# Optimization experiments

Measured on AMD Instinct MI355X. Metric: run time of the kernel, lower is better.

The kernel has to match this reference:

```python
import jax, jax.numpy as jnp
import numpy as np

N = 50000
E = 800000
D = 128          # in_dim = hid_dim = out_dim
R = 8            # num_rels
B = 8            # num_bases
N_LAYERS = 2


def _rgcn_conv(x, basis, comp, root, bias, src, dst, etype):
    """One PyG-style RGCNConv with basis decomposition, mean aggregation per
    relation, root (self-loop) weight and bias.
    x: [N, Din]; basis: [B, Din, Dout]; comp: [R, B]; root: [Din, Dout]; bias: [Dout].
    """
    n = x.shape[0]
    # Relation weights from basis decomposition: W[r] = sum_b comp[r,b] * basis[b]
    W = jnp.einsum('rb,bio->rio', comp, basis)           # [R, Din, Dout]
    # Transform every node under every relation, then gather per-edge message.
    H = jnp.einsum('ni,rio->nro', x, W)                  # [N, R, Dout]
    msg = H[src, etype]                                  # [E, Dout]
    # Per-(dst, relation) in-degree for mean aggregation (PyG aggr='mean').
    deg = jnp.zeros((n, R), x.dtype).at[dst, etype].add(1.0)
    inv = 1.0 / jnp.maximum(deg[dst, etype], 1.0)        # [E]
    agg = jnp.zeros((n, W.shape[2]), x.dtype).at[dst].add(msg * inv[:, None])
    return agg + x @ root + bias


def setup_inputs() -> dict:
    key = jax.random.key(0)
    ks = jax.random.split(key, 3 + 4 * N_LAYERS)
    x = jax.random.normal(ks[0], (N, D), dtype=jnp.float32)
    edge_index = jax.random.randint(ks[1], (2, E), 0, N, dtype=jnp.int64)
    edge_type = jax.random.randint(ks[2], (E,), 0, R, dtype=jnp.int64)
    inp = {'x': x, 'edge_index': edge_index, 'edge_type': edge_type}
    scale = 1.0 / np.sqrt(D)
    for l in range(N_LAYERS):
        k0, k1, k2 = ks[3 + 4 * l], ks[4 + 4 * l], ks[5 + 4 * l]
        inp[f'basis{l}'] = jax.random.normal(k0, (B, D, D), dtype=jnp.float32) * scale
        inp[f'comp{l}'] = jax.random.normal(k1, (R, B), dtype=jnp.float32) * (1.0 / np.sqrt(B))
        inp[f'root{l}'] = jax.random.normal(k2, (D, D), dtype=jnp.float32) * scale
        inp[f'bias{l}'] = jnp.zeros((D,), dtype=jnp.float32)
    return inp


def reference(x, edge_index, edge_type,
              basis0, comp0, root0, bias0,
              basis1, comp1, root1, bias1):
    src, dst = edge_index[0], edge_index[1]
    etype = edge_type
    h = _rgcn_conv(x, basis0, comp0, root0, bias0, src, dst, etype)
    h = jax.nn.relu(h)                 # activation between layers (dropout=0.0)
    h = _rgcn_conv(h, basis1, comp1, root1, bias1, src, dst, etype)
    return h
```

## Files before the change

### kernel.cpp

```cpp
#include <hip/hip_runtime.h>

#define NN 50000
#define EE 800000
#define DD 128
#define RR 8
#define KSTACK 1152
#define NR2 (NN * RR)
#define RPB 16
#define ROWB 2304
#define DUMPB 36864u
#define DUMP16 2304

typedef __attribute__((ext_vector_type(8))) short bf16x8;
typedef __attribute__((ext_vector_type(4))) float f32x4;

__device__ inline float bf2f(ushort u) {
    union { uint i; float f; } v; v.i = ((uint)u) << 16; return v.f;
}
__device__ inline ushort f2bf(float f) {
    uint b = __float_as_uint(f);
    uint r = (b + 0x7fffu + ((b >> 16) & 1u)) >> 16;
    return (ushort)r;
}

__global__ void __launch_bounds__(256) k_build_w3(
        const float* __restrict__ b0, const float* __restrict__ c0,
        const float* __restrict__ r0, const float* __restrict__ b1,
        const float* __restrict__ c1, const float* __restrict__ r1,
        ushort* __restrict__ w0, ushort* __restrict__ w1) {
    __shared__ float tile[32][132];
    const float* basis = blockIdx.y ? b1 : b0;
    const float* comp  = blockIdx.y ? c1 : c0;
    const float* root  = blockIdx.y ? r1 : r0;
    ushort* wT         = blockIdx.y ? w1 : w0;
    int tid = threadIdx.x;
    int k0 = blockIdx.x * 32;
    #pragma unroll
    for (int it = 0; it < 16; ++it) {
        int idx = it * 256 + tid;
        int kk = idx >> 7, o = idx & 127;
        int k = k0 + kk;
        float val;
        if (k < RR * DD) {
            int r = k >> 7, i = k & 127;
            float s = 0.f;
            #pragma unroll
            for (int b = 0; b < 8; ++b) s += comp[r * 8 + b] * basis[(b * 128 + i) * 128 + o];
            val = s;
        } else {
            val = root[(k - RR * DD) * 128 + o];
        }
        tile[kk][o] = val;
    }
    __syncthreads();
    int o = tid >> 1, half = tid & 1;
    ushort* wp = wT + (size_t)o * KSTACK + k0 + half * 16;
    #pragma unroll
    for (int j = 0; j < 8; ++j) {
        float lo = tile[half * 16 + 2 * j][o];
        float hi = tile[half * 16 + 2 * j + 1][o];
        uint pk;
        asm("v_cvt_pk_bf16_f32 %0, %1, %2" : "=v"(pk) : "v"(lo), "v"(hi));
        *(uint*)(wp + 2 * j) = pk;
    }
}

__global__ void k_cvt_bf16(const float* __restrict__ x, ushort* __restrict__ xb, int n4) {
    int i = blockIdx.x * 256 + threadIdx.x;
    if (i < n4) {
        float4 v = ((const float4*)x)[i];
        uint2 p;
        p.x = (uint)f2bf(v.x) | ((uint)f2bf(v.y) << 16);
        p.y = (uint)f2bf(v.z) | ((uint)f2bf(v.w) << 16);
        ((uint2*)xb)[i] = p;
    }
}

__global__ void k_hist(const int* __restrict__ ei, const int* __restrict__ et,
                       int* __restrict__ deg_dr) {
    int e = blockIdx.x * 256 + threadIdx.x;
    if (e < EE) atomicAdd(&deg_dr[ei[EE + e] * RR + et[e]], 1);
}

__device__ inline int rowdeg(const int* __restrict__ deg_dr, int n) {
    int4 a = ((const int4*)deg_dr)[2 * n];
    int4 b = ((const int4*)deg_dr)[2 * n + 1];
    return a.x + a.y + a.z + a.w + b.x + b.y + b.z + b.w;
}

__global__ void k_scan1(const int* __restrict__ deg_dr, int* __restrict__ bsum, int n) {
    __shared__ int s[256];
    int t = threadIdx.x;
    int i = blockIdx.x * 256 + t;
    s[t] = (i < n) ? rowdeg(deg_dr, i) : 0;
    __syncthreads();
    for (int o = 128; o > 0; o >>= 1) {
        if (t < o) s[t] += s[t + o];
        __syncthreads();
    }
    if (t == 0) bsum[blockIdx.x] = s[0];
}

__global__ void k_scan2(int* __restrict__ bsum, int nb) {
    __shared__ int s[256];
    int t = threadIdx.x;
    int v = (t < nb) ? bsum[t] : 0;
    s[t] = v;
    __syncthreads();
    for (int o = 1; o < 256; o <<= 1) {
        int u = (t >= o) ? s[t - o] : 0;
        __syncthreads();
        s[t] += u;
        __syncthreads();
    }
    if (t < nb) bsum[t] = s[t] - v;
}

__global__ void k_scan3(const int* __restrict__ deg_dr, const int* __restrict__ boff,
                        int* __restrict__ ptr, int n) {
    __shared__ int s[256];
    int t = threadIdx.x;
    int i = blockIdx.x * 256 + t;
    int v = (i < n) ? rowdeg(deg_dr, i) : 0;
    s[t] = v;
    __syncthreads();
    for (int o = 1; o < 256; o <<= 1) {
        int u = (t >= o) ? s[t - o] : 0;
        __syncthreads();
        s[t] += u;
        __syncthreads();
    }
    if (i < n) ptr[i + 1] = boff[blockIdx.x] + s[t];
    if (i == 0) ptr[0] = 0;
}

__global__ void k_scatter(const int* __restrict__ ei, const int* __restrict__ et,
                          const int* __restrict__ row_ptr, const int* __restrict__ deg_dr,
                          int* __restrict__ cursor, int2* __restrict__ ekw) {
    int e = blockIdx.x * 256 + threadIdx.x;
    if (e < EE) {
        int s = ei[e], d = ei[EE + e], t = et[e];
        int4 a = ((const int4*)deg_dr)[2 * d];
        int4 b = ((const int4*)deg_dr)[2 * d + 1];
        int pre = 0;
        pre += (t > 0) ? a.x : 0; pre += (t > 1) ? a.y : 0;
        pre += (t > 2) ? a.z : 0; pre += (t > 3) ? a.w : 0;
        pre += (t > 4) ? b.x : 0; pre += (t > 5) ? b.y : 0;
        pre += (t > 6) ? b.z : 0;
        int deg = (t == 0) ? a.x : (t == 1) ? a.y : (t == 2) ? a.z : (t == 3) ? a.w
                : (t == 4) ? b.x : (t == 5) ? b.y : (t == 6) ? b.z : b.w;
        int p = row_ptr[d] + pre + atomicAdd(&cursor[d * RR + t], 1);
        int lrow = d & (RPB - 1);
        int base16 = lrow * (ROWB >> 4) + t * 16;
        int2 pk;
        pk.x = (base16 << 19) | ((lrow & 7) << 16) | s;
        pk.y = __float_as_int(1.f / (float)deg);
        ekw[p] = pk;
    }
}

__global__ void __launch_bounds__(512, 4) k_fused8(
        const ushort* __restrict__ in, const int* __restrict__ rp,
        const int2* __restrict__ ekw, const ushort* __restrict__ BT,
        const float* __restrict__ bias, ushort* __restrict__ hout,
        float* __restrict__ fout) {
    __shared__ uint4 at4[(RPB * ROWB + 256) / 16];
    char* atb = (char*)at4;
    int tid = threadIdx.x, wid = tid >> 6, lane = tid & 63;
    int blockrow = blockIdx.x * RPB;
    uint lane4 = (uint)lane << 2;

    {
        uint4 z = {0u, 0u, 0u, 0u};
        for (int i = tid; i < (RPB * ROWB + 256) / 16; i += 512) at4[i] = z;
    }
    __syncthreads();

    const ushort* inl = in + (lane << 1);

    #pragma unroll
    for (int rr = 0; rr < 2; ++rr) {
        int lr = (wid << 1) + rr;
        int n = blockrow + lr;
        uint su = *(const uint*)(inl + (size_t)n * DD);
        uint off = (uint)(lr * ROWB + 2048) + (lane4 ^ ((uint)(lr & 7) << 4));
        *(uint*)(atb + off) = su;
    }

    int n0 = blockrow + (wid << 1);
    int p    = __builtin_amdgcn_readfirstlane(rp[n0]);
    int pend = __builtin_amdgcn_readfirstlane(rp[n0 + 2]);
    int nb = pend - p;

    const int U = 8;
    int2 kA[U], kB[U];
    uint gA[U], gB[U];
    float a0 = 0.f, a1 = 0.f;
    uint prev = 0xFFFFFFFFu;

    auto loadc = [&](int2* kb, uint* gb, int base) {
        #pragma unroll
        for (int j = 0; j < U; ++j) {
            int pe = base + j;
            bool dummy = pe >= pend;
            pe = dummy ? (pend - 1) : pe;
            int2 e = ekw[pe];
            if (dummy) { e.x = (int)((uint)DUMP16 << 19); e.y = 0; }
            kb[j] = e;
        }
        #pragma unroll
        for (int j = 0; j < U; ++j)
            gb[j] = *(const uint*)(inl + ((size_t)(kb[j].x & 0xFFFF)) * DD);
    };
    auto proc = [&](int2* kb, uint* gb) {
        #pragma unroll
        for (int j = 0; j < U; ++j) {
            uint ex = (uint)kb[j].x;
            float w = __int_as_float(kb[j].y);
            uint off = ((ex >> 19) << 4) + (lane4 ^ ((ex >> 12) & 0x70u));
            bool same = (off == prev);
            a0 = same ? a0 : 0.f;
            a1 = same ? a1 : 0.f;
            uint g = gb[j];
            a0 += w * bf2f((ushort)(g & 0xFFFFu));
            a1 += w * bf2f((ushort)(g >> 16));
            uint pk;
            asm("v_cvt_pk_bf16_f32 %0, %1, %2" : "=v"(pk) : "v"(a0), "v"(a1));
            *(uint*)(atb + off) = pk;
            prev = off;
        }
    };

    if (nb > 0) {
        int nch = (nb + U - 1) / U;
        loadc(kA, gA, p);
        int i = 1;
        for (; i + 1 < nch; i += 2) {
            loadc(kB, gB, p + i * U);
            proc(kA, gA);
            loadc(kA, gA, p + (i + 1) * U);
            proc(kB, gB);
        }
        if (i < nch) {
            loadc(kB, gB, p + i * U);
            proc(kA, gA);
            proc(kB, gB);
        } else {
            proc(kA, gA);
        }
    }
    __syncthreads();

    int rlo = lane & 15, q = lane >> 4;
    int colbase = wid << 4;
    uint x7 = (uint)(rlo & 7) << 4;
    const char* arow = atb + rlo * ROWB;
    const ushort* bp = BT + (size_t)(colbase + rlo) * KSTACK + (q << 3);
    f32x4 c0 = {0.f, 0.f, 0.f, 0.f};
    #pragma unroll 4
    for (int kk = 0; kk < KSTACK / 32; ++kk) {
        uint loff = (uint)(kk * 64 + q * 16) ^ x7;
        bf16x8 af = *(const bf16x8*)(arow + loff);
        bf16x8 b  = *(const bf16x8*)(bp + kk * 32);
        c0 = __builtin_amdgcn_mfma_f32_16x16x32_bf16(af, b, c0, 0, 0, 0);
    }
    int col = colbase + rlo;
    float bv = bias[col];
    int rowoff = q << 2;
    #pragma unroll
    for (int rg = 0; rg < 4; ++rg) {
        int row = blockrow + rowoff + rg;
        float v = c0[rg] + bv;
        if (hout) {
            v = fmaxf(v, 0.f);
            hout[(size_t)row * DD + col] = f2bf(v);
        } else {
            fout[(size_t)row * DD + col] = v;
        }
    }
}

extern "C" void kernel_launch(void* const* d_in, const int* in_sizes, int n_in,
                              void* d_out, int out_size, void* d_ws, size_t ws_size,
                              hipStream_t stream) {
    const float* x      = (const float*)d_in[0];
    const int*   ei     = (const int*)d_in[1];
    const int*   et     = (const int*)d_in[2];
    const float* basis0 = (const float*)d_in[3];
    const float* comp0  = (const float*)d_in[4];
    const float* root0  = (const float*)d_in[5];
    const float* bias0  = (const float*)d_in[6];
    const float* basis1 = (const float*)d_in[7];
    const float* comp1  = (const float*)d_in[8];
    const float* root1  = (const float*)d_in[9];
    const float* bias1  = (const float*)d_in[10];
    float* out = (float*)d_out;

    char* ws = (char*)d_ws;
    size_t off = 0;
    auto alloc = [&](size_t bytes) -> void* {
        void* p = ws + off;
        off += (bytes + 255) & ~(size_t)255;
        return p;
    };
    int*    deg_dr  = (int*)alloc((size_t)NR2 * 4);
    int*    cursor  = (int*)alloc((size_t)NR2 * 4);
    size_t zero_bytes = off;
    int*    row_ptr = (int*)alloc((size_t)(NN + 1) * 4);
    int*    bsum    = (int*)alloc(256 * 4);
    int2*   ekw     = (int2*)alloc((size_t)EE * 8);
    ushort* wT0     = (ushort*)alloc((size_t)DD * KSTACK * 2);
    ushort* wT1     = (ushort*)alloc((size_t)DD * KSTACK * 2);
    ushort* xb      = (ushort*)alloc((size_t)NN * DD * 2);
    ushort* h       = (ushort*)alloc((size_t)NN * DD * 2);
    if (off > ws_size) return;

    hipMemsetAsync(d_ws, 0, zero_bytes, stream);

    dim3 wgrid(KSTACK / 32, 2);
    k_build_w3<<<wgrid, 256, 0, stream>>>(basis0, comp0, root0, basis1, comp1, root1, wT0, wT1);
    k_cvt_bf16<<<6250, 256, 0, stream>>>(x, xb, NN * DD / 4);
    k_hist<<<3125, 256, 0, stream>>>(ei, et, deg_dr);
    k_scan1<<<196, 256, 0, stream>>>(deg_dr, bsum, NN);
    k_scan2<<<1, 256, 0, stream>>>(bsum, 196);
    k_scan3<<<196, 256, 0, stream>>>(deg_dr, bsum, row_ptr, NN);
    k_scatter<<<3125, 256, 0, stream>>>(ei, et, row_ptr, deg_dr, cursor, ekw);

    int fblocks = NN / RPB;
    k_fused8<<<fblocks, 512, 0, stream>>>(xb, row_ptr, ekw, wT0, bias0, h, nullptr);
    k_fused8<<<fblocks, 512, 0, stream>>>(h, row_ptr, ekw, wT1, bias1, nullptr, out);
}
```

Measured before the change: 339.2 us.

## Simplify edge gather loop to raise occupancy and drop initial barrier

```diff
diff --git a/kernel.cpp b/kernel.cpp
--- a/kernel.cpp
+++ b/kernel.cpp
@@ -8,8 +8,6 @@
 #define NR2 (NN * RR)
 #define RPB 16
 #define ROWB 2304
-#define DUMPB 36864u
-#define DUMP16 2304
 
 typedef __attribute__((ext_vector_type(8))) short bf16x8;
 typedef __attribute__((ext_vector_type(4))) float f32x4;
@@ -159,12 +157,12 @@
     }
 }
 
-__global__ void __launch_bounds__(512, 4) k_fused8(
+__global__ void __launch_bounds__(512, 8) k_fused9(
         const ushort* __restrict__ in, const int* __restrict__ rp,
         const int2* __restrict__ ekw, const ushort* __restrict__ BT,
         const float* __restrict__ bias, ushort* __restrict__ hout,
         float* __restrict__ fout) {
-    __shared__ uint4 at4[(RPB * ROWB + 256) / 16];
+    __shared__ uint4 at4[RPB * ROWB / 16];
     char* atb = (char*)at4;
     int tid = threadIdx.x, wid = tid >> 6, lane = tid & 63;
     int blockrow = blockIdx.x * RPB;
@@ -172,9 +170,14 @@
 
     {
         uint4 z = {0u, 0u, 0u, 0u};
-        for (int i = tid; i < (RPB * ROWB + 256) / 16; i += 512) at4[i] = z;
-    }
-    __syncthreads();
+        #pragma unroll
+        for (int r = 0; r < 2; ++r) {
+            char* zb = atb + (wid * 2 + r) * ROWB + lane * 16;
+            *(uint4*)(zb) = z;
+            *(uint4*)(zb + 1024) = z;
+            if (lane < 16) *(uint4*)(zb + 2048) = z;
+        }
+    }
 
     const ushort* inl = in + (lane << 1);
 
@@ -190,64 +193,25 @@
     int n0 = blockrow + (wid << 1);
     int p    = __builtin_amdgcn_readfirstlane(rp[n0]);
     int pend = __builtin_amdgcn_readfirstlane(rp[n0 + 2]);
-    int nb = pend - p;
-
-    const int U = 8;
-    int2 kA[U], kB[U];
-    uint gA[U], gB[U];
+
     float a0 = 0.f, a1 = 0.f;
     uint prev = 0xFFFFFFFFu;
-
-    auto loadc = [&](int2* kb, uint* gb, int base) {
-        #pragma unroll
-        for (int j = 0; j < U; ++j) {
-            int pe = base + j;
-            bool dummy = pe >= pend;
-            pe = dummy ? (pend - 1) : pe;
-            int2 e = ekw[pe];
-            if (dummy) { e.x = (int)((uint)DUMP16 << 19); e.y = 0; }
-            kb[j] = e;
-        }
-        #pragma unroll
-        for (int j = 0; j < U; ++j)
-            gb[j] = *(const uint*)(inl + ((size_t)(kb[j].x & 0xFFFF)) * DD);
-    };
-    auto proc = [&](int2* kb, uint* gb) {
-        #pragma unroll
-        for (int j = 0; j < U; ++j) {
-            uint ex = (uint)kb[j].x;
-            float w = __int_as_float(kb[j].y);
-            uint off = ((ex >> 19) << 4) + (lane4 ^ ((ex >> 12) & 0x70u));
-            bool same = (off == prev);
-            a0 = same ? a0 : 0.f;
-            a1 = same ? a1 : 0.f;
-            uint g = gb[j];
-            a0 += w * bf2f((ushort)(g & 0xFFFFu));
-            a1 += w * bf2f((ushort)(g >> 16));
-            uint pk;
-            asm("v_cvt_pk_bf16_f32 %0, %1, %2" : "=v"(pk) : "v"(a0), "v"(a1));
-            *(uint*)(atb + off) = pk;
-            prev = off;
-        }
-    };
-
-    if (nb > 0) {
-        int nch = (nb + U - 1) / U;
-        loadc(kA, gA, p);
-        int i = 1;
-        for (; i + 1 < nch; i += 2) {
-            loadc(kB, gB, p + i * U);
-            proc(kA, gA);
-            loadc(kA, gA, p + (i + 1) * U);
-            proc(kB, gB);
-        }
-        if (i < nch) {
-            loadc(kB, gB, p + i * U);
-            proc(kA, gA);
-            proc(kB, gB);
-        } else {
-            proc(kA, gA);
-        }
+    #pragma unroll 4
+    for (; p < pend; ++p) {
+        int2 e = ekw[p];
+        uint ex = (uint)e.x;
+        uint g = *(const uint*)(inl + (size_t)(ex & 0xFFFFu) * DD);
+        float w = __int_as_float(e.y);
+        uint off = ((ex >> 19) << 4) + (lane4 ^ ((ex >> 12) & 0x70u));
+        bool same = (off == prev);
+        a0 = same ? a0 : 0.f;
+        a1 = same ? a1 : 0.f;
+        a0 += w * bf2f((ushort)(g & 0xFFFFu));
+        a1 += w * bf2f((ushort)(g >> 16));
+        uint pk;
+        asm("v_cvt_pk_bf16_f32 %0, %1, %2" : "=v"(pk) : "v"(a0), "v"(a1));
+        *(uint*)(atb + off) = pk;
+        prev = off;
     }
     __syncthreads();
 
@@ -327,6 +291,6 @@
     k_scatter<<<3125, 256, 0, stream>>>(ei, et, row_ptr, deg_dr, cursor, ekw);
 
     int fblocks = NN / RPB;
-    k_fused8<<<fblocks, 512, 0, stream>>>(xb, row_ptr, ekw, wT0, bias0, h, nullptr);
-    k_fused8<<<fblocks, 512, 0, stream>>>(h, row_ptr, ekw, wT1, bias1, nullptr, out);
-}
+    k_fused9<<<fblocks, 512, 0, stream>>>(xb, row_ptr, ekw, wT0, bias0, h, nullptr);
+    k_fused9<<<fblocks, 512, 0, stream>>>(h, row_ptr, ekw, wT1, bias1, nullptr, out);
+}
```

After: 400.4 us. 1.18x slower.
